# Kernel tuning notes

Hardware: AMD Instinct MI355X
Metric: run time of the kernel (lower is better)

The kernel has to match this reference:

```python
import jax, jax.numpy as jnp
import numpy as np

N, C, H, K = 4096, 512, 128, 3
NEG = -jnp.inf


def _linear(x, W, b):
    return x @ W.T + b


def _lrelu(x):
    return jnp.where(x > 0, x, 0.01 * x)  # nn.LeakyReLU default slope


def _cos_sim(x, y):
    # torch cal_cos_similarity: xy / (|x| |y|^T), NaN (0/0) -> 0
    xy = x @ y.T
    den = jnp.linalg.norm(x, axis=1, keepdims=True) * jnp.linalg.norm(y, axis=1, keepdims=True).T
    return xy / jnp.where(den == 0, 1.0, den)


def setup_inputs() -> dict:
    key = jax.random.key(0)
    ks = jax.random.split(key, 24)
    x_hidden = jax.random.normal(ks[0], (N, H), jnp.float32)
    cm = (jax.random.uniform(ks[1], (N, C)) < 0.05).astype(jnp.float32)
    # ensure every concept has at least one member stock (no empty concepts)
    cm = cm.at[jnp.arange(C) % N, jnp.arange(C)].set(1.0)
    market_value = jax.random.uniform(ks[2], (N,), jnp.float32, 0.1, 1.0)
    s = 1.0 / np.sqrt(H)
    inp = {"x_hidden": x_hidden, "concept_matrix": cm, "market_value": market_value}
    names = ["ps", "ps_fore", "ps_back", "hs", "hs_fore", "hs_back", "indi"]
    for i, n in enumerate(names):
        inp[f"W_{n}"] = jax.random.uniform(ks[3 + 2 * i], (H, H), jnp.float32, -s, s)
        inp[f"b_{n}"] = jax.random.uniform(ks[4 + 2 * i], (H,), jnp.float32, -s, s)
    inp["W_out"] = jax.random.uniform(ks[20], (1, H), jnp.float32, -s, s)
    inp["b_out"] = jax.random.uniform(ks[21], (1,), jnp.float32, -s, s)
    return inp


def reference(x_hidden, concept_matrix, market_value,
              W_ps, b_ps, W_ps_fore, b_ps_fore, W_ps_back, b_ps_back,
              W_hs, b_hs, W_hs_fore, b_hs_fore, W_hs_back, b_hs_back,
              W_indi, b_indi, W_out, b_out):
    x = x_hidden
    n = x.shape[0]
    # --- predefined-concept (ps) branch ---
    s2c = concept_matrix * market_value[:, None]                     # [N,C]
    s2c_den = s2c.sum(0)[None, :] * concept_matrix + 1.0
    s2c = s2c / s2c_den
    hidden = s2c.T @ x                                               # [C,H]
    valid1 = hidden.sum(1) != 0                                      # row-filter mask
    s2c2 = jax.nn.softmax(x @ hidden.T, axis=0)                      # softmax over stocks
    hidden = (s2c2.T @ x) * valid1[:, None]                          # [C,H]
    c2s = jax.nn.softmax(jnp.where(valid1[None, :], _cos_sim(x, hidden), NEG), axis=1)
    p_shared = _linear(c2s @ hidden, W_ps, b_ps)
    p_back = _linear(p_shared, W_ps_back, b_ps_back)
    out_ps = _lrelu(_linear(p_shared, W_ps_fore, b_ps_fore))
    # --- hidden-concept (hs) branch ---
    h = x - p_back
    hs2c = _cos_sim(h, h)                                            # [N,N]
    diag = jnp.diagonal(hs2c)
    hs2c = hs2c * (1.0 - jnp.eye(n, dtype=h.dtype))
    idx = jax.lax.top_k(hs2c, K)[1]                                  # [N,K]
    mask = jnp.zeros((n, n), h.dtype).at[jnp.arange(n)[:, None], idx].set(1.0)
    hs2c = hs2c * mask
    hs2c = hs2c + jnp.diag((hs2c.sum(0) != 0).astype(h.dtype) * diag)
    hidden2 = hs2c.T @ h                                             # [N,H]
    valid2 = hidden2.sum(1) != 0
    hidden2 = hidden2 * valid2[:, None]
    hc2s = jax.nn.softmax(jnp.where(valid2[None, :], _cos_sim(h, hidden2), NEG), axis=1)
    h_shared = _linear(hc2s @ hidden2, W_hs, b_hs)
    h_back = _linear(h_shared, W_hs_back, b_hs_back)
    out_hs = _lrelu(_linear(h_shared, W_hs_fore, b_hs_fore))
    # --- individual branch ---
    indiv = x - p_back - h_back
    out_indi = _lrelu(_linear(indiv, W_indi, b_indi))
    all_info = out_ps + out_hs + out_indi
    return _linear(all_info, W_out, b_out).squeeze()                 # [N]
```

## Files before the change

### kernel.cpp

```cpp
#include <hip/hip_runtime.h>
#include <hip/hip_fp16.h>
#include <math.h>

#define N 4096
#define C 512
#define H 128
#define PAD 40
#define WP 136

typedef __attribute__((ext_vector_type(8))) short bf16x8;
typedef __attribute__((ext_vector_type(4))) float f32x4;


__device__ inline float wave_reduce_sum(float v) {
#pragma unroll
  for (int m = 32; m; m >>= 1) v += __shfl_xor(v, m);
  return v;
}

__device__ inline float lrelu(float v) { return v > 0.f ? v : 0.01f * v; }

__device__ inline bool better(float v, int j, float w, int k) {
  return (v > w) || (v == w && j < k);
}

__device__ inline void top3_ins(float v, int j, float& v0, int& j0,
                                float& v1, int& j1, float& v2, int& j2) {
  if (better(v, j, v0, j0)) { v2 = v1; j2 = j1; v1 = v0; j1 = j0; v0 = v; j0 = j; }
  else if (better(v, j, v1, j1)) { v2 = v1; j2 = j1; v1 = v; j1 = j; }
  else if (better(v, j, v2, j2)) { v2 = v; j2 = j; }
}

__device__ inline void ins5(float s, int j, float v[5], int jx[5]) {
  if (!better(s, j, v[4], jx[4])) return;
  if (better(s, j, v[0], jx[0])) {
    v[4]=v[3]; jx[4]=jx[3]; v[3]=v[2]; jx[3]=jx[2]; v[2]=v[1]; jx[2]=jx[1];
    v[1]=v[0]; jx[1]=jx[0]; v[0]=s; jx[0]=j;
  } else if (better(s, j, v[1], jx[1])) {
    v[4]=v[3]; jx[4]=jx[3]; v[3]=v[2]; jx[3]=jx[2]; v[2]=v[1]; jx[2]=jx[1];
    v[1]=s; jx[1]=j;
  } else if (better(s, j, v[2], jx[2])) {
    v[4]=v[3]; jx[4]=jx[3]; v[3]=v[2]; jx[3]=jx[2]; v[2]=s; jx[2]=j;
  } else if (better(s, j, v[3], jx[3])) {
    v[4]=v[3]; jx[4]=jx[3]; v[3]=s; jx[3]=j;
  } else {
    v[4]=s; jx[4]=j;
  }
}

__device__ inline unsigned short f2bf(float f) {
  unsigned u = __float_as_uint(f);
  unsigned r = u + 0x7fffu + ((u >> 16) & 1u);
  return (unsigned short)(r >> 16);
}
__device__ inline float bf2f(unsigned short h) {
  return __uint_as_float(((unsigned)h) << 16);
}

__global__ __launch_bounds__(256) void k_split(const float* __restrict__ in,
                                               unsigned short* __restrict__ hi,
                                               unsigned short* __restrict__ lo,
                                               float* __restrict__ nrm) {
  int t = threadIdx.x;
  int idx = (blockIdx.x * 256 + t) * 4;
  float4 v = *(const float4*)&in[idx];
  float vv[4] = {v.x, v.y, v.z, v.w};
  unsigned short h[4], l[4];
  float ss = 0.f;
#pragma unroll
  for (int c = 0; c < 4; c++) {
    ss += vv[c] * vv[c];
    h[c] = f2bf(vv[c]);
    l[c] = f2bf(vv[c] - bf2f(h[c]));
  }
  uint2 ph = {(unsigned)h[0] | ((unsigned)h[1] << 16),
              (unsigned)h[2] | ((unsigned)h[3] << 16)};
  uint2 pl = {(unsigned)l[0] | ((unsigned)l[1] << 16),
              (unsigned)l[2] | ((unsigned)l[3] << 16)};
  *(uint2*)&hi[idx] = ph;
  *(uint2*)&lo[idx] = pl;
  if (nrm) {
#pragma unroll
    for (int m = 16; m; m >>= 1) ss += __shfl_xor(ss, m);
    if ((t & 31) == 0) nrm[idx >> 7] = sqrtf(ss);
  }
}

__global__ __launch_bounds__(256) void k_tsplit(const float* __restrict__ in,
                                                unsigned short* __restrict__ thi,
                                                unsigned short* __restrict__ tlo,
                                                int R) {
// ... 40 lines not shown

__global__ __launch_bounds__(256) void k_colstats(const float* __restrict__ sc,
                                                  float* __restrict__ colmax,
                                                  float* __restrict__ colsum) {
  __shared__ float red[256];
  int c = blockIdx.x, t = threadIdx.x;
  float v[16];
  float m = -3e38f;
#pragma unroll
  for (int q = 0; q < 16; q++) {
    v[q] = sc[(size_t)(q * 256 + t) * C + c];
    m = fmaxf(m, v[q]);
  }
  red[t] = m; __syncthreads();
  for (int s = 128; s; s >>= 1) { if (t < s) red[t] = fmaxf(red[t], red[t + s]); __syncthreads(); }
  m = red[0]; __syncthreads();
  float sum = 0.f;
#pragma unroll
  for (int q = 0; q < 16; q++) sum += __expf(v[q] - m);
  red[t] = sum; __syncthreads();
  for (int s = 128; s; s >>= 1) { if (t < s) red[t] += red[t + s]; __syncthreads(); }
  if (t == 0) { colmax[c] = m; colsum[c] = red[0]; }
}

__global__ __launch_bounds__(256) void k_cs_softmax(
    const float* __restrict__ sc, const float* __restrict__ xnorm,
    const float* __restrict__ hnorm, const float* __restrict__ valid1,
    unsigned short* __restrict__ cshi, unsigned short* __restrict__ cslo) {
  __shared__ float red[256];
  int i = blockIdx.x, t = threadIdx.x;
  float xn = xnorm[i];
  float r0 = sc[(size_t)i * C + t], r1 = sc[(size_t)i * C + 256 + t];
  float d0 = xn * hnorm[t], d1 = xn * hnorm[256 + t];
  float c0 = r0 / (d0 == 0.f ? 1.f : d0);
  float c1 = r1 / (d1 == 0.f ? 1.f : d1);
  float s0 = (valid1[t] != 0.f) ? c0 : -3e38f;
  float s1 = (valid1[256 + t] != 0.f) ? c1 : -3e38f;
  red[t] = fmaxf(s0, s1); __syncthreads();
  for (int s = 128; s; s >>= 1) { if (t < s) red[t] = fmaxf(red[t], red[t + s]); __syncthreads(); }
  float m = red[0]; __syncthreads();
  float p0 = (s0 > -1e37f) ? __expf(s0 - m) : 0.f;
  float p1 = (s1 > -1e37f) ? __expf(s1 - m) : 0.f;
  red[t] = p0 + p1; __syncthreads();
  for (int s = 128; s; s >>= 1) { if (t < s) red[t] += red[t + s]; __syncthreads(); }
  float inv = 1.f / red[0];
  float a = p0 * inv, b = p1 * inv;
  unsigned short ha = f2bf(a), hb = f2bf(b);
  cshi[(size_t)i * C + t] = ha;
  cslo[(size_t)i * C + t] = f2bf(a - bf2f(ha));
  cshi[(size_t)i * C + 256 + t] = hb;
  cslo[(size_t)i * C + 256 + t] = f2bf(b - bf2f(hb));
}

__global__ __launch_bounds__(64) void k_fin_hidden2(
    const float* __restrict__ h, const float* __restrict__ diagv,
    const float* __restrict__ colsum_m, float* __restrict__ hidden2,
    unsigned short* __restrict__ h2hi, unsigned short* __restrict__ h2lo,
    float* __restrict__ valid2f) {
  int j = blockIdx.x, t = threadIdx.x;
  float add = (colsum_m[j] != 0.f) ? diagv[j] : 0.f;
  float a = hidden2[(size_t)j * H + t] + add * h[(size_t)j * H + t];
  float b = hidden2[(size_t)j * H + 64 + t] + add * h[(size_t)j * H + 64 + t];
  float s = a + b, ss = a * a + b * b;
#pragma unroll
  for (int m = 32; m; m >>= 1) { s += __shfl_xor(s, m); ss += __shfl_xor(ss, m); }
  bool valid = (s != 0.f);
  a = valid ? a : 0.f; b = valid ? b : 0.f;
  hidden2[(size_t)j * H + t] = a;
  hidden2[(size_t)j * H + 64 + t] = b;
  float inv = (valid && ss > 0.f) ? (1.f / sqrtf(ss)) : 1.f;
  float va = a * inv, vb = b * inv;
  unsigned short ha = f2bf(va), hb = f2bf(vb);
  h2hi[(size_t)j * H + t] = ha;
  h2lo[(size_t)j * H + t] = f2bf(va - bf2f(ha));
  h2hi[(size_t)j * H + 64 + t] = hb;
  h2lo[(size_t)j * H + 64 + t] = f2bf(vb - bf2f(hb));
  if (t == 0) valid2f[j] = valid ? 1.f : 0.f;
}

template <int EPI>
__global__ __launch_bounds__(256) void k_mfma_nt(
    const unsigned short* __restrict__ Ahi, const unsigned short* __restrict__ Alo,
    const unsigned short* __restrict__ Bhi, const unsigned short* __restrict__ Blo,
    const float* __restrict__ validn, float* __restrict__ out,
    unsigned short* __restrict__ ehi, float* __restrict__ lsum, int Nn) {
  __shared__ __align__(16) unsigned short sAh[128 * PAD];
  __shared__ __align__(16) unsigned short sAl[128 * PAD];
  __shared__ __align__(16) unsigned short sBh[128 * PAD];
  __shared__ __align__(16) unsigned short sBl[128 * PAD];
  int tid = threadIdx.x;
  int bm = blockIdx.y * 128, bn = blockIdx.x * 128;
  int lane = tid & 63, w = tid >> 6;
  int wm = (w & 1) * 64, wn = (w >> 1) * 64;
  int l15 = lane & 15, quad = lane >> 4;
  f32x4 zero = {0.f, 0.f, 0.f, 0.f};
  f32x4 acc[4][4];
#pragma unroll
  for (int mt = 0; mt < 4; mt++)
#pragma unroll
    for (int nt = 0; nt < 4; nt++) acc[mt][nt] = zero;

  for (int kt = 0; kt < 128; kt += 32) {
#pragma unroll
    for (int q = 0; q < 2; q++) {
      int f = tid * 2 + q;
      int row = f >> 2, ch = f & 3;
      size_t ga = (size_t)(bm + row) * 128 + kt + ch * 8;
      size_t gb = (size_t)(bn + row) * 128 + kt + ch * 8;
      int ls = row * PAD + ch * 8;
      *(uint4*)&sAh[ls] = *(const uint4*)&Ahi[ga];
      *(uint4*)&sAl[ls] = *(const uint4*)&Alo[ga];
      *(uint4*)&sBh[ls] = *(const uint4*)&Bhi[gb];
      *(uint4*)&sBl[ls] = *(const uint4*)&Blo[gb];
    }
    __syncthreads();
    bf16x8 ah[4], al[4], bh[4], bl[4];
#pragma unroll
    for (int t = 0; t < 4; t++) {
      int ar = (wm + t * 16 + l15) * PAD + quad * 8;
      ah[t] = *(const bf16x8*)&sAh[ar];
      al[t] = *(const bf16x8*)&sAl[ar];
      int br = (wn + t * 16 + l15) * PAD + quad * 8;
      bh[t] = *(const bf16x8*)&sBh[br];
      bl[t] = *(const bf16x8*)&sBl[br];
    }
#pragma unroll
    for (int mt = 0; mt < 4; mt++)
#pragma unroll
      for (int nt = 0; nt < 4; nt++) {
        acc[mt][nt] = __builtin_amdgcn_mfma_f32_16x16x32_bf16(ah[mt], bh[nt], acc[mt][nt], 0, 0, 0);
        acc[mt][nt] = __builtin_amdgcn_mfma_f32_16x16x32_bf16(ah[mt], bl[nt], acc[mt][nt], 0, 0, 0);
        acc[mt][nt] = __builtin_amdgcn_mfma_f32_16x16x32_bf16(al[mt], bh[nt], acc[mt][nt], 0, 0, 0);
      }
    __syncthreads();
  }
  if (EPI == 3) {
    float vm[4];
#pragma unroll
    for (int nt = 0; nt < 4; nt++) vm[nt] = validn[bn + wn + nt * 16 + l15];
#pragma unroll
    for (int mt = 0; mt < 4; mt++) {
#pragma unroll
      for (int rg = 0; rg < 4; rg++) {
        int row = bm + wm + mt * 16 + quad * 4 + rg;
        float rsum = 0.f;
#pragma unroll
        for (int nt = 0; nt < 4; nt++) {
          int col = bn + wn + nt * 16 + l15;
          float e = (vm[nt] != 0.f) ? __expf(acc[mt][nt][rg] - 1.f) : 0.f;
          rsum += e;
          ehi[(size_t)row * N + col] = f2bf(e);
        }
#pragma unroll
        for (int d = 1; d < 16; d <<= 1) rsum += __shfl_xor(rsum, d);
        if (l15 == 0) atomicAdd(&lsum[row], rsum);
      }
    }
  } else if (EPI == 2) {
#pragma unroll
    for (int mt = 0; mt < 4; mt++) {
#pragma unroll
      for (int nt = 0; nt < 4; nt++) {
        int col = bn + wn + nt * 16 + l15;
#pragma unroll
        for (int rg = 0; rg < 4; rg++) {
          int row = bm + wm + mt * 16 + quad * 4 + rg;
          float v = (row == col) ? 0.f : acc[mt][nt][rg];
          ehi[(size_t)row * N + col] = __half_as_ushort(__float2half(v));
        }
      }
    }
  } else {
#pragma unroll
    for (int mt = 0; mt < 4; mt++) {
#pragma unroll
      for (int nt = 0; nt < 4; nt++) {
        int col = bn + wn + nt * 16 + l15;
#pragma unroll
        for (int rg = 0; rg < 4; rg++) {
          int row = bm + wm + mt * 16 + quad * 4 + rg;
          out[(size_t)row * Nn + col] = acc[mt][nt][rg];
        }
      }
    }
  }
}

__global__ __launch_bounds__(256) void k_rowtop(
    const unsigned short* __restrict__ Sh, const float* __restrict__ hhat,
    float* __restrict__ mtv, int* __restrict__ mtj) {
  int i = blockIdx.x * 4 + (threadIdx.x >> 6);
  int lane = threadIdx.x & 63;
  const unsigned short* row = &Sh[(size_t)i * N];
  float v[5] = {-3e38f, -3e38f, -3e38f, -3e38f, -3e38f};
  int jx[5] = {0x7fffffff, 0x7fffffff, 0x7fffffff, 0x7fffffff, 0x7fffffff};
  for (int t = 0; t < 8; t++) {
    int base = t * 512 + lane * 8;
    uint4 p = *(const uint4*)&row[base];
    unsigned pk[4] = {p.x, p.y, p.z, p.w};
#pragma unroll
    for (int c = 0; c < 4; c++) {
      float e0 = __half2float(__ushort_as_half((unsigned short)(pk[c] & 0xffffu)));
      float e1 = __half2float(__ushort_as_half((unsigned short)(pk[c] >> 16)));
      ins5(e0, base + c * 2, v, jx);
      ins5(e1, base + c * 2 + 1, v, jx);
    }
  }
#pragma unroll
  for (int d = 1; d < 64; d <<= 1) {
    float fv[5]; int fj[5];
#pragma unroll
    for (int c = 0; c < 5; c++) { fv[c] = __shfl_xor(v[c], d); fj[c] = __shfl_xor(jx[c], d); }
#pragma unroll
    for (int c = 0; c < 5; c++) ins5(fv[c], fj[c], v, jx);
  }
  const float* hi = &hhat[(size_t)i * H];
  float b0 = -3e38f, b1 = -3e38f, b2 = -3e38f;
  int q0 = 0, q1 = 0, q2 = 0;
#pragma unroll
  for (int c = 0; c < 5; c++) {
    int j = jx[c];
    float s;
    if (j == i) {
      s = 0.f;
    } else {
      const float* hj = &hhat[(size_t)j * H];
      float p = hi[lane] * hj[lane] + hi[lane + 64] * hj[lane + 64];
      s = wave_reduce_sum(p);
    }
    top3_ins(s, j, b0, q0, b1, q1, b2, q2);
  }
  if (lane == 0) {
    mtv[i * 3 + 0] = b0; mtv[i * 3 + 1] = b1; mtv[i * 3 + 2] = b2;
    mtj[i * 3 + 0] = q0; mtj[i * 3 + 1] = q1; mtj[i * 3 + 2] = q2;
  }
}

template <int ALO>
__global__ __launch_bounds__(256) void k_mfma_kn(
    const unsigned short* __restrict__ Ahi, const unsigned short* __restrict__ Alo,
    const unsigned short* __restrict__ Bthi, const unsigned short* __restrict__ Btlo,
    float* __restrict__ partial, int lda, int KC) {
  __shared__ __align__(16) unsigned short sAh[128 * PAD];
  __shared__ __align__(16) unsigned short sAl[128 * PAD];
  __shared__ __align__(16) unsigned short sBh[128 * PAD];
  __shared__ __align__(16) unsigned short sBl[128 * PAD];
  int tid = threadIdx.x;
  int bm = blockIdx.y * 128;
  int k0 = blockIdx.z * KC;
  int lane = tid & 63, w = tid >> 6;
  int wm = (w & 1) * 64, wn = (w >> 1) * 64;
  int l15 = lane & 15, quad = lane >> 4;
  f32x4 zero = {0.f, 0.f, 0.f, 0.f};
  f32x4 acc[4][4];
#pragma unroll
  for (int mt = 0; mt < 4; mt++)
#pragma unroll
    for (int nt = 0; nt < 4; nt++) acc[mt][nt] = zero;

  for (int kt = 0; kt < KC; kt += 32) {
#pragma unroll
    for (int q = 0; q < 2; q++) {
      int f = tid * 2 + q;
      int row = f >> 2, ch = f & 3;
      size_t ga = (size_t)(bm + row) * lda + k0 + kt + ch * 8;
      size_t gb = (size_t)row * lda + k0 + kt + ch * 8;
      int ls = row * PAD + ch * 8;
      *(uint4*)&sAh[ls] = *(const uint4*)&Ahi[ga];
      if (ALO) *(uint4*)&sAl[ls] = *(const uint4*)&Alo[ga];
      *(uint4*)&sBh[ls] = *(const uint4*)&Bthi[gb];
      *(uint4*)&sBl[ls] = *(const uint4*)&Btlo[gb];
    }
    __syncthreads();
    bf16x8 ah[4], al[4], bh[4], bl[4];
#pragma unroll
    for (int t = 0; t < 4; t++) {
      int ar = (wm + t * 16 + l15) * PAD + quad * 8;
      ah[t] = *(const bf16x8*)&sAh[ar];
      if (ALO) al[t] = *(const bf16x8*)&sAl[ar];
      int br = (wn + t * 16 + l15) * PAD + quad * 8;
      bh[t] = *(const bf16x8*)&sBh[br];
      bl[t] = *(const bf16x8*)&sBl[br];
    }
#pragma unroll
    for (int mt = 0; mt < 4; mt++)
#pragma unroll
      for (int nt = 0; nt < 4; nt++) {
        acc[mt][nt] = __builtin_amdgcn_mfma_f32_16x16x32_bf16(ah[mt], bh[nt], acc[mt][nt], 0, 0, 0);
        acc[mt][nt] = __builtin_amdgcn_mfma_f32_16x16x32_bf16(ah[mt], bl[nt], acc[mt][nt], 0, 0, 0);
        if (ALO)
          acc[mt][nt] = __builtin_amdgcn_mfma_f32_16x16x32_bf16(al[mt], bh[nt], acc[mt][nt], 0, 0, 0);
      }
    __syncthreads();
  }
  float* pp = partial + (size_t)blockIdx.z * N * 128;
#pragma unroll
  for (int mt = 0; mt < 4; mt++)
#pragma unroll
    for (int nt = 0; nt < 4; nt++) {
      int col = wn + nt * 16 + l15;
#pragma unroll
      for (int rg = 0; rg < 4; rg++) {
        int row = bm + wm + mt * 16 + quad * 4 + rg;
        pp[(size_t)row * 128 + col] = acc[mt][nt][rg];
      }
    }
}

template <int AMODE>
__global__ __launch_bounds__(256) void k_mfma_genA(
    const float* __restrict__ P, const float* __restrict__ mv,
    const float* __restrict__ col1, const float* __restrict__ col2,
    const unsigned short* __restrict__ Bthi, const unsigned short* __restrict__ Btlo,
    float* __restrict__ partial, int KC) {
  __shared__ __align__(16) unsigned short sAh[128 * PAD];
  __shared__ __align__(16) unsigned short sAl[128 * PAD];
  __shared__ __align__(16) unsigned short sBh[128 * PAD];
  __shared__ __align__(16) unsigned short sBl[128 * PAD];
  int tid = threadIdx.x;
  int bm = blockIdx.y * 128;
  int k0 = blockIdx.z * KC;
  int lane = tid & 63, w = tid >> 6;
  int wm = (w & 1) * 64, wn = (w >> 1) * 64;
  int l15 = lane & 15, quad = lane >> 4;
  f32x4 zero = {0.f, 0.f, 0.f, 0.f};
  f32x4 acc[4][4];
#pragma unroll
  for (int mt = 0; mt < 4; mt++)
#pragma unroll
    for (int nt = 0; nt < 4; nt++) acc[mt][nt] = zero;

  for (int kt = 0; kt < KC; kt += 32) {
    int kr = tid >> 3;
    int mc = (tid & 7) * 16;
    int k = k0 + kt + kr;
    float mvk = (AMODE == 1) ? mv[k] : 0.f;
#pragma unroll
    for (int q = 0; q < 4; q++) {
      int m0 = mc + q * 4;
      float4 pv = *(const float4*)&P[(size_t)k * C + bm + m0];
      float4 c1 = *(const float4*)&col1[bm + m0];
      float wv[4];
      if (AMODE == 1) {
        wv[0] = pv.x * mvk / (c1.x * pv.x + 1.f);
        wv[1] = pv.y * mvk / (c1.y * pv.y + 1.f);
        wv[2] = pv.z * mvk / (c1.z * pv.z + 1.f);
        wv[3] = pv.w * mvk / (c1.w * pv.w + 1.f);
      } else {
        float4 c2 = *(const float4*)&col2[bm + m0];
        wv[0] = __expf(pv.x - c1.x) / c2.x;
        wv[1] = __expf(pv.y - c1.y) / c2.y;
        wv[2] = __expf(pv.z - c1.z) / c2.z;
        wv[3] = __expf(pv.w - c1.w) / c2.w;
      }
#pragma unroll
      for (int j = 0; j < 4; j++) {
        unsigned short hh = f2bf(wv[j]);
        sAh[(m0 + j) * PAD + kr] = hh;
        sAl[(m0 + j) * PAD + kr] = f2bf(wv[j] - bf2f(hh));
      }
    }
#pragma unroll
    for (int q = 0; q < 2; q++) {
      int f = q * 256 + tid;
      int row = f >> 2, ch = f & 3;
      size_t gb = (size_t)row * N + k0 + kt + ch * 8;
      int ls = row * PAD + ch * 8;
      *(uint4*)&sBh[ls] = *(const uint4*)&Bthi[gb];
      *(uint4*)&sBl[ls] = *(const uint4*)&Btlo[gb];
    }
    __syncthreads();
    bf16x8 ah[4], al[4], bh[4], bl[4];
#pragma unroll
    for (int t = 0; t < 4; t++) {
      int ar = (wm + t * 16 + l15) * PAD + quad * 8;
      ah[t] = *(const bf16x8*)&sAh[ar];
      al[t] = *(const bf16x8*)&sAl[ar];
      int br = (wn + t * 16 + l15) * PAD + quad * 8;
      bh[t] = *(const bf16x8*)&sBh[br];
      bl[t] = *(const bf16x8*)&sBl[br];
    }
#pragma unroll
    for (int mt = 0; mt < 4; mt++)
#pragma unroll
      for (int nt = 0; nt < 4; nt++) {
        acc[mt][nt] = __builtin_amdgcn_mfma_f32_16x16x32_bf16(ah[mt], bh[nt], acc[mt][nt], 0, 0, 0);
        acc[mt][nt] = __builtin_amdgcn_mfma_f32_16x16x32_bf16(ah[mt], bl[nt], acc[mt][nt], 0, 0, 0);
        acc[mt][nt] = __builtin_amdgcn_mfma_f32_16x16x32_bf16(al[mt], bh[nt], acc[mt][nt], 0, 0, 0);
      }
    __syncthreads();
  }
  float* pp = partial + (size_t)blockIdx.z * C * 128;
#pragma unroll
  for (int mt = 0; mt < 4; mt++)
#pragma unroll
    for (int nt = 0; nt < 4; nt++) {
      int col = wn + nt * 16 + l15;
#pragma unroll
      for (int rg = 0; rg < 4; rg++) {
        int row = bm + wm + mt * 16 + quad * 4 + rg;
        pp[(size_t)row * 128 + col] = acc[mt][nt][rg];
      }
    }
}

__global__ __launch_bounds__(256) void k_scatter(
    const float* __restrict__ mtv, const int* __restrict__ mtj,
    const float* __restrict__ h, float* __restrict__ hidden2,
    float* __restrict__ colsum_m) {
  int i = blockIdx.x * 4 + (threadIdx.x >> 6);
  int lane = threadIdx.x & 63;
  float h0 = h[(size_t)i * H + lane], h1 = h[(size_t)i * H + 64 + lane];
#pragma unroll
  for (int s = 0; s < 3; s++) {
    float v = mtv[i * 3 + s];
    int j = mtj[i * 3 + s];
    atomicAdd(&hidden2[(size_t)j * H + lane], v * h0);
    atomicAdd(&hidden2[(size_t)j * H + 64 + lane], v * h1);
    if (lane == s) atomicAdd(&colsum_m[j], v);
  }
}

__global__ __launch_bounds__(256) void k_reduce(
    const float* __restrict__ partial, float* __restrict__ out, int cnt,
    size_t slot, size_t size4, const float* __restrict__ scalem,
    const float* __restrict__ divm, unsigned short* __restrict__ hi,
    unsigned short* __restrict__ lo, float* __restrict__ nrmout,
    float* __restrict__ validout) {
  size_t idx = (size_t)blockIdx.x * 256 + threadIdx.x;
  if (idx >= size4) return;
  float4 s = {0, 0, 0, 0};
  for (int c = 0; c < cnt; c++) {
    float4 v = *(const float4*)&partial[c * slot + idx * 4];
    s.x += v.x; s.y += v.y; s.z += v.z; s.w += v.w;
  }
  if (scalem) {
    float sc = scalem[idx >> 5];
    s.x *= sc; s.y *= sc; s.z *= sc; s.w *= sc;
  }
  if (divm) {
    float sc = 1.f / divm[idx >> 5];
    s.x *= sc; s.y *= sc; s.z *= sc; s.w *= sc;
  }
  *(float4*)&out[idx * 4] = s;
  if (hi) {
    float vv[4] = {s.x, s.y, s.z, s.w};
    unsigned short h[4], l[4];
#pragma unroll
    for (int c = 0; c < 4; c++) {
      h[c] = f2bf(vv[c]);
      l[c] = f2bf(vv[c] - bf2f(h[c]));
    }
    uint2 ph = {(unsigned)h[0] | ((unsigned)h[1] << 16),
                (unsigned)h[2] | ((unsigned)h[3] << 16)};
    uint2 pl = {(unsigned)l[0] | ((unsigned)l[1] << 16),
                (unsigned)l[2] | ((unsigned)l[3] << 16)};
    *(uint2*)&hi[idx * 4] = ph;
    *(uint2*)&lo[idx * 4] = pl;
  }
  if (nrmout || validout) {
    float rs = s.x + s.y + s.z + s.w;
    float rq = s.x * s.x + s.y * s.y + s.z * s.z + s.w * s.w;
#pragma unroll
    for (int m = 16; m; m >>= 1) { rs += __shfl_xor(rs, m); rq += __shfl_xor(rq, m); }
    if ((threadIdx.x & 31) == 0) {
      if (nrmout) nrmout[idx >> 5] = sqrtf(rq);
      if (validout) validout[idx >> 5] = (rs != 0.f) ? 1.f : 0.f;
    }
  }
}


#define LOAD_W(Wt)                                                        \
  do {                                                                    \
    _Pragma("unroll") for (int q = 0; q < 16; q++) {                      \
      int f = q * 256 + tid;                                              \
      int wr = f >> 5, wc = (f & 31) * 4;                                 \
      float4 wv = *(const float4*)&(Wt)[(size_t)wr * 128 + wc];           \
      float ww[4] = {wv.x, wv.y, wv.z, wv.w};                             \
      _Pragma("unroll") for (int c = 0; c < 4; c++) {                     \
        unsigned short hh = f2bf(ww[c]);                                  \
        sWh[wr * WP + wc + c] = hh;                                       \
        sWl[wr * WP + wc + c] = f2bf(ww[c] - bf2f(hh));                   \
      }                                                                   \
    }                                                                     \
  } while (0)

#define GEMM32(accv)                                                              \
  do {                                                                            \
    _Pragma("unroll") for (int nt = 0; nt < 4; nt++) accv[nt] = zero;             \
    _Pragma("unroll") for (int kt = 0; kt < 128; kt += 32) {                      \
      bf16x8 ah = *(const bf16x8*)&sAh[(rt + l15) * WP + kt + quad * 8];          \
      bf16x8 al = *(const bf16x8*)&sAl[(rt + l15) * WP + kt + quad * 8];          \
      _Pragma("unroll") for (int nt = 0; nt < 4; nt++) {                          \
        int br = (ch2 + nt * 16 + l15) * WP + kt + quad * 8;                      \
        bf16x8 bh = *(const bf16x8*)&sWh[br];                                     \
        bf16x8 bl = *(const bf16x8*)&sWl[br];                                     \
        accv[nt] = __builtin_amdgcn_mfma_f32_16x16x32_bf16(ah, bh, accv[nt], 0, 0, 0); \
        accv[nt] = __builtin_amdgcn_mfma_f32_16x16x32_bf16(ah, bl, accv[nt], 0, 0, 0); \
        accv[nt] = __builtin_amdgcn_mfma_f32_16x16x32_bf16(al, bh, accv[nt], 0, 0, 0); \
      }                                                                           \
    }                                                                             \
  } while (0)

__global__ __launch_bounds__(256) void k_ps_tail(
    const float* __restrict__ A, const float* __restrict__ x,
    const float* __restrict__ W_ps, const float* __restrict__ b_ps,
    const float* __restrict__ W_psb, const float* __restrict__ b_psb,
    const float* __restrict__ W_psf, const float* __restrict__ b_psf,
    float* __restrict__ hbuf, float* __restrict__ hhat,
    unsigned short* __restrict__ hhi, unsigned short* __restrict__ hlo,
    float* __restrict__ diagv, float* __restrict__ all_info) {
  __shared__ __align__(16) unsigned short sWh[128 * WP];
  __shared__ __align__(16) unsigned short sWl[128 * WP];
  __shared__ __align__(16) unsigned short sAh[32 * WP];
  __shared__ __align__(16) unsigned short sAl[32 * WP];
  __shared__ __align__(16) float sF[32][132];
  int tid = threadIdx.x;
  int bm = blockIdx.x * 32;
  int lane = tid & 63, w = tid >> 6;
  int rt = (w & 1) * 16, ch2 = (w >> 1) * 64;
  int l15 = lane & 15, quad = lane >> 4;
  f32x4 zero = {0.f, 0.f, 0.f, 0.f};
  f32x4 acc[4];
// ... 155 lines not shown
    float bv = b_hs[col];
#pragma unroll
    for (int rg = 0; rg < 4; rg++) {
      int row = rt + quad * 4 + rg;
      float v = acc[nt][rg] + bv;
      unsigned short hh = f2bf(v);
      sAh[row * WP + col] = hh;
      sAl[row * WP + col] = f2bf(v - bf2f(hh));
    }
  }
  LOAD_W(W_hsf);
  __syncthreads();
  GEMM32(acc);
#pragma unroll
  for (int nt = 0; nt < 4; nt++) {
    int col = ch2 + nt * 16 + l15;
    float bv = b_hsf[col];
#pragma unroll
    for (int rg = 0; rg < 4; rg++) {
      int row = rt + quad * 4 + rg;
      size_t off = (size_t)(bm + row) * 128 + col;
      allv[nt][rg] = all_info[off] + lrelu(acc[nt][rg] + bv);
    }
  }
  __syncthreads();
  LOAD_W(W_hsb);
  __syncthreads();
  GEMM32(acc);
  float iv[4][4];
#pragma unroll
  for (int nt = 0; nt < 4; nt++) {
    int col = ch2 + nt * 16 + l15;
    float bv = b_hsb[col];
#pragma unroll
    for (int rg = 0; rg < 4; rg++) {
      int row = rt + quad * 4 + rg;
      size_t off = (size_t)(bm + row) * 128 + col;
      iv[nt][rg] = hbuf[off] - (acc[nt][rg] + bv);
    }
  }
  __syncthreads();
#pragma unroll
  for (int nt = 0; nt < 4; nt++) {
    int col = ch2 + nt * 16 + l15;
#pragma unroll
    for (int rg = 0; rg < 4; rg++) {
      int row = rt + quad * 4 + rg;
      unsigned short hh = f2bf(iv[nt][rg]);
      sAh[row * WP + col] = hh;
      sAl[row * WP + col] = f2bf(iv[nt][rg] - bf2f(hh));
    }
  }
  LOAD_W(W_in);
  __syncthreads();
  GEMM32(acc);
#pragma unroll
  for (int nt = 0; nt < 4; nt++) {
    int col = ch2 + nt * 16 + l15;
    float bv = b_in[col];
#pragma unroll
    for (int rg = 0; rg < 4; rg++) {
      int row = rt + quad * 4 + rg;
      allv[nt][rg] += lrelu(acc[nt][rg] + bv);
      sF[row][col] = allv[nt][rg];
    }
  }
  __syncthreads();
  {
    int row = tid >> 3, c0 = (tid & 7) * 16;
    float s = 0.f;
#pragma unroll
    for (int q = 0; q < 16; q++) s += sF[row][c0 + q] * W_out[c0 + q];
    s += __shfl_xor(s, 1);
    s += __shfl_xor(s, 2);
    s += __shfl_xor(s, 4);
    if ((tid & 7) == 0) out[bm + row] = s + b_out[0];
  }
}


extern "C" void kernel_launch(void* const* d_in, const int* in_sizes, int n_in,
                              void* d_out, int out_size, void* d_ws, size_t ws_size,
                              hipStream_t stream) {
  (void)in_sizes; (void)n_in; (void)out_size;
  const float* x   = (const float*)d_in[0];
  const float* cm  = (const float*)d_in[1];
  const float* mv  = (const float*)d_in[2];
  const float* W_ps = (const float*)d_in[3],  *b_ps = (const float*)d_in[4];
  const float* W_psf = (const float*)d_in[5], *b_psf = (const float*)d_in[6];
  const float* W_psb = (const float*)d_in[7], *b_psb = (const float*)d_in[8];
  const float* W_hs = (const float*)d_in[9],  *b_hs = (const float*)d_in[10];
  const float* W_hsf = (const float*)d_in[11], *b_hsf = (const float*)d_in[12];
  const float* W_hsb = (const float*)d_in[13], *b_hsb = (const float*)d_in[14];
  const float* W_in = (const float*)d_in[15], *b_in = (const float*)d_in[16];
  const float* W_out = (const float*)d_in[17], *b_out = (const float*)d_in[18];
  float* out = (float*)d_out;

  float* W = (float*)d_ws;
  size_t o = 0;
  auto alloc = [&](size_t n) { float* p = W + o; o += n; return p; };
  float* colsum_c = alloc(C);
  float* colmax   = alloc(C);
  float* colsumexp= alloc(C);
  float* valid1   = alloc(C);
  float* hnorm_ps = alloc(C);
  float* xnorm    = alloc(N);
  float* diagv    = alloc(N);
  float* colsum_m = alloc(N);
  float* valid2f  = alloc(N);
  float* lsum     = alloc(N);
  float* mtv      = alloc(3 * N);
  int*   mtj      = (int*)alloc(3 * N);
  float* hidden1  = alloc((size_t)C * H);
  float* hidden_ps= alloc((size_t)C * H);
  float* scores   = alloc((size_t)N * C);
  float* ps_pre   = alloc((size_t)N * H);
  float* all_info = alloc((size_t)N * H);
  float* hbuf     = alloc((size_t)N * H);
  float* hhat     = alloc((size_t)N * H);
  float* hidden2  = alloc((size_t)N * H);
  unsigned short* xhi    = (unsigned short*)alloc((size_t)N * H / 2);
  unsigned short* xlo    = (unsigned short*)alloc((size_t)N * H / 2);
  unsigned short* hhathi = (unsigned short*)alloc((size_t)N * H / 2);
  unsigned short* hhatlo = (unsigned short*)alloc((size_t)N * H / 2);
  unsigned short* h2hi   = (unsigned short*)alloc((size_t)N * H / 2);
  unsigned short* h2lo   = (unsigned short*)alloc((size_t)N * H / 2);
  unsigned short* h1hi   = (unsigned short*)alloc((size_t)C * H / 2);
  unsigned short* h1lo   = (unsigned short*)alloc((size_t)C * H / 2);
  unsigned short* hpshi  = (unsigned short*)alloc((size_t)C * H / 2);
  unsigned short* hpslo  = (unsigned short*)alloc((size_t)C * H / 2);
  unsigned short* cshi   = (unsigned short*)alloc((size_t)N * C / 2);
  unsigned short* cslo   = (unsigned short*)alloc((size_t)N * C / 2);
  unsigned short* hpst_hi= (unsigned short*)alloc((size_t)H * C / 2);
  unsigned short* hpst_lo= (unsigned short*)alloc((size_t)H * C / 2);
  unsigned short* h2t_hi = (unsigned short*)alloc((size_t)H * N / 2);
  unsigned short* h2t_lo = (unsigned short*)alloc((size_t)H * N / 2);
  unsigned short* xt_hi  = (unsigned short*)alloc((size_t)H * N / 2);
  unsigned short* xt_lo  = (unsigned short*)alloc((size_t)H * N / 2);
  float* Sbuf     = alloc((size_t)N * N / 2);
  unsigned short* Sh  = (unsigned short*)Sbuf;
  unsigned short* Ehi = (unsigned short*)Sbuf;
  float* partial  = W + o;
  size_t rem = ws_size / 4 - o;
  int Z = (rem >= (size_t)16 * N * H) ? 16 : 8;
  int KC = 4096 / Z;

  hipMemsetAsync(colsum_c, 0, C * sizeof(float), stream);
  hipMemsetAsync(colsum_m, 0, N * sizeof(float), stream);
  hipMemsetAsync(lsum, 0, N * sizeof(float), stream);
  hipMemsetAsync(hidden2, 0, (size_t)N * H * sizeof(float), stream);

  dim3 blk(256);
  k_split<<<dim3(N * H / 1024), blk, 0, stream>>>(x, xhi, xlo, xnorm);
  k_tsplit<<<dim3(N / 32), blk, 0, stream>>>(x, xt_hi, xt_lo, N);
  k_colsum_s2c<<<dim3(C / 64, 16), dim3(64), 0, stream>>>(cm, mv, colsum_c);
  k_mfma_genA<1><<<dim3(1, C / 128, 32), blk, 0, stream>>>(
      cm, mv, colsum_c, nullptr, xt_hi, xt_lo, partial, N / 32);
  k_reduce<<<dim3(C * H / 4 / 256), blk, 0, stream>>>(
      partial, hidden1, 32, (size_t)C * H, (size_t)C * H / 4, nullptr, nullptr,
      h1hi, h1lo, nullptr, valid1);
  k_mfma_nt<0><<<dim3(C / 128, N / 128), blk, 0, stream>>>(
      xhi, xlo, h1hi, h1lo, nullptr, scores, nullptr, nullptr, C);
  k_colstats<<<dim3(C), blk, 0, stream>>>(scores, colmax, colsumexp);
  k_mfma_genA<2><<<dim3(1, C / 128, 32), blk, 0, stream>>>(
      scores, nullptr, colmax, colsumexp, xt_hi, xt_lo, partial, N / 32);
  k_reduce<<<dim3(C * H / 4 / 256), blk, 0, stream>>>(
      partial, hidden_ps, 32, (size_t)C * H, (size_t)C * H / 4, valid1, nullptr,
      hpshi, hpslo, hnorm_ps, nullptr);
  k_mfma_nt<0><<<dim3(C / 128, N / 128), blk, 0, stream>>>(
      xhi, xlo, hpshi, hpslo, nullptr, scores, nullptr, nullptr, C);
  k_cs_softmax<<<dim3(N), blk, 0, stream>>>(scores, xnorm, hnorm_ps, valid1,
                                            cshi, cslo);
  k_tsplit<<<dim3(C / 32), blk, 0, stream>>>(hidden_ps, hpst_hi, hpst_lo, C);
  k_mfma_kn<1><<<dim3(1, N / 128, 4), blk, 0, stream>>>(
      cshi, cslo, hpst_hi, hpst_lo, partial, C, C / 4);
  k_reduce<<<dim3(N * H / 4 / 256), blk, 0, stream>>>(
      partial, ps_pre, 4, (size_t)N * H, (size_t)N * H / 4, nullptr, nullptr,
      nullptr, nullptr, nullptr, nullptr);
  k_ps_tail<<<dim3(N / 32), blk, 0, stream>>>(
      ps_pre, x, W_ps, b_ps, W_psb, b_psb, W_psf, b_psf,
      hbuf, hhat, hhathi, hhatlo, diagv, all_info);
  k_mfma_nt<2><<<dim3(N / 128, N / 128), blk, 0, stream>>>(
      hhathi, hhatlo, hhathi, hhatlo, nullptr, nullptr, Sh, nullptr, N);
  k_rowtop<<<dim3(N / 4), blk, 0, stream>>>(Sh, hhat, mtv, mtj);
  k_scatter<<<dim3(N / 4), blk, 0, stream>>>(mtv, mtj, hbuf, hidden2, colsum_m);
  k_fin_hidden2<<<dim3(N), dim3(64), 0, stream>>>(hbuf, diagv, colsum_m, hidden2,
                                                  h2hi, h2lo, valid2f);
  k_mfma_nt<3><<<dim3(N / 128, N / 128), blk, 0, stream>>>(
      hhathi, hhatlo, h2hi, h2lo, valid2f, nullptr, Ehi, lsum, N);
  k_tsplit<<<dim3(N / 32), blk, 0, stream>>>(hidden2, h2t_hi, h2t_lo, N);
  k_mfma_kn<0><<<dim3(1, N / 128, Z), blk, 0, stream>>>(
      Ehi, nullptr, h2t_hi, h2t_lo, partial, N, KC);
  k_reduce<<<dim3(N * H / 4 / 256), blk, 0, stream>>>(
      partial, ps_pre, Z, (size_t)N * H, (size_t)N * H / 4, nullptr, lsum,
      nullptr, nullptr, nullptr, nullptr);
  k_hs_tail<<<dim3(N / 32), blk, 0, stream>>>(
      ps_pre, hbuf, all_info, W_hs, b_hs, W_hsf, b_hsf, W_hsb, b_hsb,
      W_in, b_in, W_out, b_out, out);
}
```

Measured before the change: 388.1 us.

## Fuse top-k candidate selection into similarity GEMM and flash-style softmax-matmul

The similarity GEMM epilogue now reduces each 64-column slice to top-5 candidates per row and writes those, instead of storing the full NxN fp16 matrix for a separate row scan. The exp-scores GEMM and the following P@V GEMM are merged into one flash-style kernel that keeps the probability tile in shared memory and writes per-split partial sums and row sums. Both changes aim to remove the round trip of the NxN intermediate through global memory. In exchange, the flash kernel does the QK and PV GEMMs serially per block with more shared memory and lower occupancy, and the split count is fixed at 8.

```diff
diff --git a/kernel.cpp b/kernel.cpp
--- a/kernel.cpp
+++ b/kernel.cpp
@@ -7,6 +7,7 @@
 #define H 128
 #define PAD 40
 #define WP 136
+#define FWP 136
 
 typedef __attribute__((ext_vector_type(8))) short bf16x8;
 typedef __attribute__((ext_vector_type(4))) float f32x4;
@@ -213,8 +214,7 @@
 __global__ __launch_bounds__(256) void k_mfma_nt(
     const unsigned short* __restrict__ Ahi, const unsigned short* __restrict__ Alo,
     const unsigned short* __restrict__ Bhi, const unsigned short* __restrict__ Blo,
-    const float* __restrict__ validn, float* __restrict__ out,
-    unsigned short* __restrict__ ehi, float* __restrict__ lsum, int Nn) {
+    float* __restrict__ out, float2* __restrict__ cand, int Nn) {
   __shared__ __align__(16) unsigned short sAh[128 * PAD];
   __shared__ __align__(16) unsigned short sAl[128 * PAD];
   __shared__ __align__(16) unsigned short sBh[128 * PAD];
@@ -265,39 +265,33 @@
       }
     __syncthreads();
   }
-  if (EPI == 3) {
-    float vm[4];
-#pragma unroll
-    for (int nt = 0; nt < 4; nt++) vm[nt] = validn[bn + wn + nt * 16 + l15];
+  if (EPI == 2) {
+    int slot = (bn >> 6) + (wn >> 6);
 #pragma unroll
     for (int mt = 0; mt < 4; mt++) {
 #pragma unroll
       for (int rg = 0; rg < 4; rg++) {
         int row = bm + wm + mt * 16 + quad * 4 + rg;
-        float rsum = 0.f;
+        float v5[5] = {-3e38f, -3e38f, -3e38f, -3e38f, -3e38f};
+        int j5[5] = {0x7fffffff, 0x7fffffff, 0x7fffffff, 0x7fffffff, 0x7fffffff};
 #pragma unroll
         for (int nt = 0; nt < 4; nt++) {
           int col = bn + wn + nt * 16 + l15;
-          float e = (vm[nt] != 0.f) ? __expf(acc[mt][nt][rg] - 1.f) : 0.f;
-          rsum += e;
-          ehi[(size_t)row * N + col] = f2bf(e);
+          float v = (row == col) ? 0.f : acc[mt][nt][rg];
+          ins5(v, col, v5, j5);
         }
 #pragma unroll
-        for (int d = 1; d < 16; d <<= 1) rsum += __shfl_xor(rsum, d);
-        if (l15 == 0) atomicAdd(&lsum[row], rsum);
-      }
-    }
-  } else if (EPI == 2) {
-#pragma unroll
-    for (int mt = 0; mt < 4; mt++) {
-#pragma unroll
-      for (int nt = 0; nt < 4; nt++) {
-        int col = bn + wn + nt * 16 + l15;
-#pragma unroll
-        for (int rg = 0; rg < 4; rg++) {
-          int row = bm + wm + mt * 16 + quad * 4 + rg;
-          float v = (row == col) ? 0.f : acc[mt][nt][rg];
-          ehi[(size_t)row * N + col] = __half_as_ushort(__float2half(v));
+        for (int d = 1; d < 16; d <<= 1) {
+          float fv[5]; int fj[5];
+#pragma unroll
+          for (int c = 0; c < 5; c++) { fv[c] = __shfl_xor(v5[c], d); fj[c] = __shfl_xor(j5[c], d); }
+#pragma unroll
+          for (int c = 0; c < 5; c++) ins5(fv[c], fj[c], v5, j5);
+        }
+        if (l15 == 0) {
+          float2* cp = &cand[((size_t)row * 64 + slot) * 5];
+#pragma unroll
+          for (int c = 0; c < 5; c++) cp[c] = {v5[c], __int_as_float(j5[c])};
         }
       }
     }
@@ -317,25 +311,18 @@
   }
 }
 
-__global__ __launch_bounds__(256) void k_rowtop(
-    const unsigned short* __restrict__ Sh, const float* __restrict__ hhat,
+__global__ __launch_bounds__(256) void k_rowtop2(
+    const float2* __restrict__ cand, const float* __restrict__ hhat,
     float* __restrict__ mtv, int* __restrict__ mtj) {
   int i = blockIdx.x * 4 + (threadIdx.x >> 6);
   int lane = threadIdx.x & 63;
-  const unsigned short* row = &Sh[(size_t)i * N];
+  const float2* cr = &cand[(size_t)i * 320];
   float v[5] = {-3e38f, -3e38f, -3e38f, -3e38f, -3e38f};
   int jx[5] = {0x7fffffff, 0x7fffffff, 0x7fffffff, 0x7fffffff, 0x7fffffff};
-  for (int t = 0; t < 8; t++) {
-    int base = t * 512 + lane * 8;
-    uint4 p = *(const uint4*)&row[base];
-    unsigned pk[4] = {p.x, p.y, p.z, p.w};
-#pragma unroll
-    for (int c = 0; c < 4; c++) {
-      float e0 = __half2float(__ushort_as_half((unsigned short)(pk[c] & 0xffffu)));
-      float e1 = __half2float(__ushort_as_half((unsigned short)(pk[c] >> 16)));
-      ins5(e0, base + c * 2, v, jx);
-      ins5(e1, base + c * 2 + 1, v, jx);
-    }
+#pragma unroll
+  for (int c = 0; c < 5; c++) {
+    float2 p = cr[lane * 5 + c];
+    ins5(p.x, __float_as_int(p.y), v, jx);
   }
 #pragma unroll
   for (int d = 1; d < 64; d <<= 1) {
@@ -367,7 +354,147 @@
   }
 }
 
-template <int ALO>
+__global__ __launch_bounds__(256) void k_flash(
+    const unsigned short* __restrict__ Qhi, const unsigned short* __restrict__ Qlo,
+    const unsigned short* __restrict__ Khi, const unsigned short* __restrict__ Klo,
+    const unsigned short* __restrict__ Vthi, const unsigned short* __restrict__ Vtlo,
+    const float* __restrict__ valid2f, float* __restrict__ partialU,
+    float* __restrict__ plsum, int KVC) {
+  __shared__ __align__(16) unsigned short sQh[128 * FWP];
+  __shared__ __align__(16) unsigned short sQl[128 * FWP];
+  __shared__ __align__(16) unsigned short sP[128 * FWP];
+  __shared__ __align__(16) unsigned short sKh[128 * PAD];
+  __shared__ __align__(16) unsigned short sKl[128 * PAD];
+  __shared__ __align__(16) unsigned short sVh[128 * PAD];
+  __shared__ __align__(16) unsigned short sVl[128 * PAD];
+  __shared__ float lsum_s[128];
+  int tid = threadIdx.x;
+  int z = blockIdx.x;
+  int bm = blockIdx.y * 128;
+  int j0 = z * KVC;
+  int lane = tid & 63, w = tid >> 6;
+  int wm = (w & 1) * 64, wn = (w >> 1) * 64;
+  int l15 = lane & 15, quad = lane >> 4;
+#pragma unroll
+  for (int q = 0; q < 8; q++) {
+    int f = q * 256 + tid;
+    int row = f >> 4, ch = f & 15;
+    size_t ga = (size_t)(bm + row) * 128 + ch * 8;
+    int ls = row * FWP + ch * 8;
+    *(uint4*)&sQh[ls] = *(const uint4*)&Qhi[ga];
+    *(uint4*)&sQl[ls] = *(const uint4*)&Qlo[ga];
+  }
+  if (tid < 128) lsum_s[tid] = 0.f;
+  __syncthreads();
+  f32x4 zero = {0.f, 0.f, 0.f, 0.f};
+  f32x4 uacc[4][4];
+#pragma unroll
+  for (int mt = 0; mt < 4; mt++)
+#pragma unroll
+    for (int nt = 0; nt < 4; nt++) uacc[mt][nt] = zero;
+
+  for (int jb = j0; jb < j0 + KVC; jb += 128) {
+    float vm[4];
+#pragma unroll
+    for (int nt = 0; nt < 4; nt++) vm[nt] = valid2f[jb + wn + nt * 16 + l15];
+    f32x4 qacc[4][4];
+#pragma unroll
+    for (int mt = 0; mt < 4; mt++)
+#pragma unroll
+      for (int nt = 0; nt < 4; nt++) qacc[mt][nt] = zero;
+    for (int kt = 0; kt < 128; kt += 32) {
+#pragma unroll
+      for (int q = 0; q < 2; q++) {
+        int f = tid * 2 + q;
+        int row = f >> 2, ch = f & 3;
+        size_t gb = (size_t)(jb + row) * 128 + kt + ch * 8;
+        int ls = row * PAD + ch * 8;
+        *(uint4*)&sKh[ls] = *(const uint4*)&Khi[gb];
+        *(uint4*)&sKl[ls] = *(const uint4*)&Klo[gb];
+      }
+      __syncthreads();
+      bf16x8 ah[4], al[4], bh[4], bl[4];
+#pragma unroll
+      for (int t = 0; t < 4; t++) {
+        int ar = (wm + t * 16 + l15) * FWP + kt + quad * 8;
+        ah[t] = *(const bf16x8*)&sQh[ar];
+        al[t] = *(const bf16x8*)&sQl[ar];
+        int br = (wn + t * 16 + l15) * PAD + quad * 8;
+        bh[t] = *(const bf16x8*)&sKh[br];
+        bl[t] = *(const bf16x8*)&sKl[br];
+      }
+#pragma unroll
+      for (int mt = 0; mt < 4; mt++)
+#pragma unroll
+        for (int nt = 0; nt < 4; nt++) {
+          qacc[mt][nt] = __builtin_amdgcn_mfma_f32_16x16x32_bf16(ah[mt], bh[nt], qacc[mt][nt], 0, 0, 0);
+          qacc[mt][nt] = __builtin_amdgcn_mfma_f32_16x16x32_bf16(ah[mt], bl[nt], qacc[mt][nt], 0, 0, 0);
+          qacc[mt][nt] = __builtin_amdgcn_mfma_f32_16x16x32_bf16(al[mt], bh[nt], qacc[mt][nt], 0, 0, 0);
+        }
+      __syncthreads();
+    }
+#pragma unroll
+    for (int mt = 0; mt < 4; mt++) {
+#pragma unroll
+      for (int rg = 0; rg < 4; rg++) {
+        int row = wm + mt * 16 + quad * 4 + rg;
+        float rs = 0.f;
+#pragma unroll
+        for (int nt = 0; nt < 4; nt++) {
+          float e = (vm[nt] != 0.f) ? __expf(qacc[mt][nt][rg] - 1.f) : 0.f;
+          rs += e;
+          sP[row * FWP + wn + nt * 16 + l15] = f2bf(e);
+        }
+#pragma unroll
+        for (int d = 1; d < 16; d <<= 1) rs += __shfl_xor(rs, d);
+        if (l15 == 0) atomicAdd(&lsum_s[row], rs);
+      }
+    }
+    for (int kt = 0; kt < 128; kt += 32) {
+#pragma unroll
+      for (int q = 0; q < 2; q++) {
+        int f = tid * 2 + q;
+        int row = f >> 2, ch = f & 3;
+        size_t gv = (size_t)row * N + jb + kt + ch * 8;
+        int ls = row * PAD + ch * 8;
+        *(uint4*)&sVh[ls] = *(const uint4*)&Vthi[gv];
+        *(uint4*)&sVl[ls] = *(const uint4*)&Vtlo[gv];
+      }
+      __syncthreads();
+      bf16x8 pa[4], vh[4], vl[4];
+#pragma unroll
+      for (int t = 0; t < 4; t++) {
+        int ar = (wm + t * 16 + l15) * FWP + kt + quad * 8;
+        pa[t] = *(const bf16x8*)&sP[ar];
+        int br = (wn + t * 16 + l15) * PAD + quad * 8;
+        vh[t] = *(const bf16x8*)&sVh[br];
+        vl[t] = *(const bf16x8*)&sVl[br];
+      }
+#pragma unroll
+      for (int mt = 0; mt < 4; mt++)
+#pragma unroll
+        for (int nt = 0; nt < 4; nt++) {
+          uacc[mt][nt] = __builtin_amdgcn_mfma_f32_16x16x32_bf16(pa[mt], vh[nt], uacc[mt][nt], 0, 0, 0);
+          uacc[mt][nt] = __builtin_amdgcn_mfma_f32_16x16x32_bf16(pa[mt], vl[nt], uacc[mt][nt], 0, 0, 0);
+        }
+      __syncthreads();
+    }
+  }
+  float* pU = partialU + (size_t)z * N * 128;
+#pragma unroll
+  for (int mt = 0; mt < 4; mt++)
+#pragma unroll
+    for (int nt = 0; nt < 4; nt++) {
+      int col = wn + nt * 16 + l15;
+#pragma unroll
+      for (int rg = 0; rg < 4; rg++) {
+        int row = bm + wm + mt * 16 + quad * 4 + rg;
+        pU[(size_t)row * 128 + col] = uacc[mt][nt][rg];
+      }
+    }
+  if (tid < 128) plsum[(size_t)z * N + bm + tid] = lsum_s[tid];
+}
+
 __global__ __launch_bounds__(256) void k_mfma_kn(
     const unsigned short* __restrict__ Ahi, const unsigned short* __restrict__ Alo,
     const unsigned short* __restrict__ Bthi, const unsigned short* __restrict__ Btlo,
@@ -398,7 +525,7 @@
       size_t gb = (size_t)row * lda + k0 + kt + ch * 8;
       int ls = row * PAD + ch * 8;
       *(uint4*)&sAh[ls] = *(const uint4*)&Ahi[ga];
-      if (ALO) *(uint4*)&sAl[ls] = *(const uint4*)&Alo[ga];
+      *(uint4*)&sAl[ls] = *(const uint4*)&Alo[ga];
       *(uint4*)&sBh[ls] = *(const uint4*)&Bthi[gb];
       *(uint4*)&sBl[ls] = *(const uint4*)&Btlo[gb];
     }
@@ -408,7 +535,7 @@
     for (int t = 0; t < 4; t++) {
       int ar = (wm + t * 16 + l15) * PAD + quad * 8;
       ah[t] = *(const bf16x8*)&sAh[ar];
-      if (ALO) al[t] = *(const bf16x8*)&sAl[ar];
+      al[t] = *(const bf16x8*)&sAl[ar];
       int br = (wn + t * 16 + l15) * PAD + quad * 8;
       bh[t] = *(const bf16x8*)&sBh[br];
       bl[t] = *(const bf16x8*)&sBl[br];
@@ -419,8 +546,7 @@
       for (int nt = 0; nt < 4; nt++) {
         acc[mt][nt] = __builtin_amdgcn_mfma_f32_16x16x32_bf16(ah[mt], bh[nt], acc[mt][nt], 0, 0, 0);
         acc[mt][nt] = __builtin_amdgcn_mfma_f32_16x16x32_bf16(ah[mt], bl[nt], acc[mt][nt], 0, 0, 0);
-        if (ALO)
-          acc[mt][nt] = __builtin_amdgcn_mfma_f32_16x16x32_bf16(al[mt], bh[nt], acc[mt][nt], 0, 0, 0);
+        acc[mt][nt] = __builtin_amdgcn_mfma_f32_16x16x32_bf16(al[mt], bh[nt], acc[mt][nt], 0, 0, 0);
       }
     __syncthreads();
   }
@@ -555,7 +681,7 @@
 __global__ __launch_bounds__(256) void k_reduce(
     const float* __restrict__ partial, float* __restrict__ out, int cnt,
     size_t slot, size_t size4, const float* __restrict__ scalem,
-    const float* __restrict__ divm, unsigned short* __restrict__ hi,
+    const float* __restrict__ plsum, unsigned short* __restrict__ hi,
     unsigned short* __restrict__ lo, float* __restrict__ nrmout,
     float* __restrict__ validout) {
   size_t idx = (size_t)blockIdx.x * 256 + threadIdx.x;
@@ -569,8 +695,11 @@
     float sc = scalem[idx >> 5];
     s.x *= sc; s.y *= sc; s.z *= sc; s.w *= sc;
   }
-  if (divm) {
-    float sc = 1.f / divm[idx >> 5];
+  if (plsum) {
+    int r = idx >> 5;
+    float d = 0.f;
+    for (int c = 0; c < cnt; c++) d += plsum[(size_t)c * N + r];
+    float sc = 1.f / d;
     s.x *= sc; s.y *= sc; s.z *= sc; s.w *= sc;
   }
   *(float4*)&out[idx * 4] = s;
@@ -892,7 +1021,7 @@
 extern "C" void kernel_launch(void* const* d_in, const int* in_sizes, int n_in,
                               void* d_out, int out_size, void* d_ws, size_t ws_size,
                               hipStream_t stream) {
-  (void)in_sizes; (void)n_in; (void)out_size;
+  (void)in_sizes; (void)n_in; (void)out_size; (void)ws_size;
   const float* x   = (const float*)d_in[0];
   const float* cm  = (const float*)d_in[1];
   const float* mv  = (const float*)d_in[2];
@@ -918,7 +1047,7 @@
   float* diagv    = alloc(N);
   float* colsum_m = alloc(N);
   float* valid2f  = alloc(N);
-  float* lsum     = alloc(N);
+  float* plsum    = alloc((size_t)8 * N);
   float* mtv      = alloc(3 * N);
   int*   mtj      = (int*)alloc(3 * N);
   float* hidden1  = alloc((size_t)C * H);
@@ -947,17 +1076,12 @@
   unsigned short* h2t_lo = (unsigned short*)alloc((size_t)H * N / 2);
   unsigned short* xt_hi  = (unsigned short*)alloc((size_t)H * N / 2);
   unsigned short* xt_lo  = (unsigned short*)alloc((size_t)H * N / 2);
-  float* Sbuf     = alloc((size_t)N * N / 2);
-  unsigned short* Sh  = (unsigned short*)Sbuf;
-  unsigned short* Ehi = (unsigned short*)Sbuf;
+  float2* cand    = (float2*)alloc((size_t)N * 64 * 5 * 2);
   float* partial  = W + o;
-  size_t rem = ws_size / 4 - o;
-  int Z = (rem >= (size_t)16 * N * H) ? 16 : 8;
-  int KC = 4096 / Z;
+  const int Z = 8;
 
   hipMemsetAsync(colsum_c, 0, C * sizeof(float), stream);
   hipMemsetAsync(colsum_m, 0, N * sizeof(float), stream);
-  hipMemsetAsync(lsum, 0, N * sizeof(float), stream);
   hipMemsetAsync(hidden2, 0, (size_t)N * H * sizeof(float), stream);
 
   dim3 blk(256);
@@ -970,7 +1094,7 @@
       partial, hidden1, 32, (size_t)C * H, (size_t)C * H / 4, nullptr, nullptr,
       h1hi, h1lo, nullptr, valid1);
   k_mfma_nt<0><<<dim3(C / 128, N / 128), blk, 0, stream>>>(
-      xhi, xlo, h1hi, h1lo, nullptr, scores, nullptr, nullptr, C);
+      xhi, xlo, h1hi, h1lo, scores, nullptr, C);
   k_colstats<<<dim3(C), blk, 0, stream>>>(scores, colmax, colsumexp);
   k_mfma_genA<2><<<dim3(1, C / 128, 32), blk, 0, stream>>>(
       scores, nullptr, colmax, colsumexp, xt_hi, xt_lo, partial, N / 32);
@@ -978,11 +1102,11 @@
       partial, hidden_ps, 32, (size_t)C * H, (size_t)C * H / 4, valid1, nullptr,
       hpshi, hpslo, hnorm_ps, nullptr);
   k_mfma_nt<0><<<dim3(C / 128, N / 128), blk, 0, stream>>>(
-      xhi, xlo, hpshi, hpslo, nullptr, scores, nullptr, nullptr, C);
+      xhi, xlo, hpshi, hpslo, scores, nullptr, C);
   k_cs_softmax<<<dim3(N), blk, 0, stream>>>(scores, xnorm, hnorm_ps, valid1,
                                             cshi, cslo);
   k_tsplit<<<dim3(C / 32), blk, 0, stream>>>(hidden_ps, hpst_hi, hpst_lo, C);
-  k_mfma_kn<1><<<dim3(1, N / 128, 4), blk, 0, stream>>>(
+  k_mfma_kn<<<dim3(1, N / 128, 4), blk, 0, stream>>>(
       cshi, cslo, hpst_hi, hpst_lo, partial, C, C / 4);
   k_reduce<<<dim3(N * H / 4 / 256), blk, 0, stream>>>(
       partial, ps_pre, 4, (size_t)N * H, (size_t)N * H / 4, nullptr, nullptr,
@@ -991,18 +1115,17 @@
       ps_pre, x, W_ps, b_ps, W_psb, b_psb, W_psf, b_psf,
       hbuf, hhat, hhathi, hhatlo, diagv, all_info);
   k_mfma_nt<2><<<dim3(N / 128, N / 128), blk, 0, stream>>>(
-      hhathi, hhatlo, hhathi, hhatlo, nullptr, nullptr, Sh, nullptr, N);
-  k_rowtop<<<dim3(N / 4), blk, 0, stream>>>(Sh, hhat, mtv, mtj);
+      hhathi, hhatlo, hhathi, hhatlo, nullptr, cand, N);
+  k_rowtop2<<<dim3(N / 4), blk, 0, stream>>>(cand, hhat, mtv, mtj);
   k_scatter<<<dim3(N / 4), blk, 0, stream>>>(mtv, mtj, hbuf, hidden2, colsum_m);
   k_fin_hidden2<<<dim3(N), dim3(64), 0, stream>>>(hbuf, diagv, colsum_m, hidden2,
                                                   h2hi, h2lo, valid2f);
-  k_mfma_nt<3><<<dim3(N / 128, N / 128), blk, 0, stream>>>(
-      hhathi, hhatlo, h2hi, h2lo, valid2f, nullptr, Ehi, lsum, N);
   k_tsplit<<<dim3(N / 32), blk, 0, stream>>>(hidden2, h2t_hi, h2t_lo, N);
-  k_mfma_kn<0><<<dim3(1, N / 128, Z), blk, 0, stream>>>(
-      Ehi, nullptr, h2t_hi, h2t_lo, partial, N, KC);
+  k_flash<<<dim3(Z, N / 128), blk, 0, stream>>>(
+      hhathi, hhatlo, h2hi, h2lo, h2t_hi, h2t_lo, valid2f, partial, plsum,
+      N / Z);
   k_reduce<<<dim3(N * H / 4 / 256), blk, 0, stream>>>(
-      partial, ps_pre, Z, (size_t)N * H, (size_t)N * H / 4, nullptr, lsum,
+      partial, ps_pre, Z, (size_t)N * H, (size_t)N * H / 4, nullptr, plsum,
       nullptr, nullptr, nullptr, nullptr);
   k_hs_tail<<<dim3(N / 32), blk, 0, stream>>>(
       ps_pre, hbuf, all_info, W_hs, b_hs, W_hsf, b_hsf, W_hsb, b_hsb,
```

After: 484.2 us. +24.8%, slower.
